# Kernel tuning notes

Hardware: AMD Instinct MI355X
Metric: run time of the kernel (lower is better)

The kernel has to match this reference:

```python
import jax, jax.numpy as jnp
import numpy as np

N_NODES = 100000
N_EDGES = 1600000
IN_F = 128
OUT_F = 128
EDGE_F = 16


def setup_inputs() -> dict:
    key = jax.random.key(0)
    ks = jax.random.split(key, 8)
    H = jax.random.normal(ks[0], (N_NODES, IN_F), dtype=jnp.float32)
    edge_index = jax.random.randint(ks[1], (2, N_EDGES), 0, N_ODES_ := N_NODES, dtype=jnp.int64) if False else jax.random.randint(ks[1], (2, N_EDGES), 0, N_NODES, dtype=jnp.int32).astype(jnp.int64)
    edge_attr = jax.random.normal(ks[2], (N_EDGES, EDGE_F), dtype=jnp.float32)
    We = jax.random.normal(ks[3], (EDGE_F, IN_F), dtype=jnp.float32) * (1.0 / np.sqrt(EDGE_F))
    be = jnp.zeros((IN_F,), dtype=jnp.float32)
    W1 = jax.random.normal(ks[4], (IN_F, OUT_F), dtype=jnp.float32) * (1.0 / np.sqrt(IN_F))
    b1 = jnp.zeros((OUT_F,), dtype=jnp.float32)
    W2 = jax.random.normal(ks[5], (OUT_F, OUT_F), dtype=jnp.float32) * (1.0 / np.sqrt(OUT_F))
    b2 = jnp.zeros((OUT_F,), dtype=jnp.float32)
    return {"H": H, "edge_index": edge_index, "edge_attr": edge_attr,
            "We": We, "be": be, "W1": W1, "b1": b1, "W2": W2, "b2": b2}


def reference(H, edge_index, edge_attr, We, be, W1, b1, W2, b2):
    # edge_mlp: Linear(edge_attr_dim -> in_features)
    edge_messages = edge_attr @ We + be                       # [E, in_f]
    # gather by src, add edge messages
    messages = H[edge_index[0]] + edge_messages               # [E, in_f]
    # scatter_add by dst with dim_size = N
    aggregated = jax.ops.segment_sum(messages, edge_index[1], num_segments=H.shape[0])  # [N, in_f]
    # node_mlp: Linear -> ReLU -> Linear
    h = jax.nn.relu(aggregated @ W1 + b1)                     # [N, out_f]
    out = h @ W2 + b2                                         # [N, out_f]
    return out
```

## Files before the change

kernel.cpp:

```cpp
#include <hip/hip_runtime.h>

#define IN_F 128
#define EF 16

typedef short bf16x8 __attribute__((ext_vector_type(8)));
typedef float f32x4  __attribute__((ext_vector_type(4)));

__device__ __forceinline__ unsigned short f2b(float f) {
    unsigned b = __float_as_uint(f);
    b += 0x7fffu + ((b >> 16) & 1u);
    return (unsigned short)(b >> 16);
}
__device__ __forceinline__ float blo(unsigned u) { return __uint_as_float(u << 16); }
__device__ __forceinline__ float bhi(unsigned u) { return __uint_as_float(u & 0xffff0000u); }


__global__ __launch_bounds__(256) void pre_kernel(
    const float* __restrict__ H, unsigned short* __restrict__ Hb, int n4,
    const int* __restrict__ ei, int* __restrict__ counts,
    int* __restrict__ rank, int E,
    const float* __restrict__ W1, unsigned short* __restrict__ W1t,
    const float* __restrict__ W2, unsigned short* __restrict__ W2t,
    int h2b_blocks, int hist_blocks)
{
    int b = blockIdx.x;
    if (b < h2b_blocks) {
        int i = b * 256 + threadIdx.x;
        if (i < n4) {
            float4 v = ((const float4*)H)[i];
            ushort4 r;
            r.x = f2b(v.x); r.y = f2b(v.y); r.z = f2b(v.z); r.w = f2b(v.w);
            ((ushort4*)Hb)[i] = r;
        }
    } else if (b < h2b_blocks + hist_blocks) {
        int e = (b - h2b_blocks) * 256 + threadIdx.x;
        if (e < E) rank[e] = atomicAdd(&counts[ei[E + e]], 1);
    } else {
        int idx = (b - h2b_blocks - hist_blocks) * 256 + threadIdx.x;
        int w = idx >> 14;
        int r = idx & 16383;
        int n = r >> 7, k = r & 127;
        if (w == 0) W1t[n * IN_F + k] = f2b(W1[k * IN_F + n]);
        else        W2t[n * IN_F + k] = f2b(W2[k * IN_F + n]);
    }
}

__global__ __launch_bounds__(256) void hist_kernel(
    const int* __restrict__ ei, int* __restrict__ counts,
    int* __restrict__ rank, int E)
{
    int e = blockIdx.x * 256 + threadIdx.x;
    if (e >= E) return;
    rank[e] = atomicAdd(&counts[ei[E + e]], 1);
}

__global__ __launch_bounds__(256) void scan_blocks_kernel(
    const int* __restrict__ in, int* __restrict__ out,
    int* __restrict__ partials, int n)
{
    __shared__ int sdata[256];
    const int t = threadIdx.x;
    const int idx0 = blockIdx.x * 1024 + t * 4;
    int v[4];
    #pragma unroll
    for (int i = 0; i < 4; i++) { int idx = idx0 + i; v[i] = (idx < n) ? in[idx] : 0; }
    int s = v[0] + v[1] + v[2] + v[3];
    sdata[t] = s;
    __syncthreads();
    for (int off = 1; off < 256; off <<= 1) {
        int x = (t >= off) ? sdata[t - off] : 0;
        __syncthreads();
        sdata[t] += x;
        __syncthreads();
    }
    if (t == 255) partials[blockIdx.x] = sdata[255];
    int run = (t > 0) ? sdata[t - 1] : 0;
    #pragma unroll
    for (int i = 0; i < 4; i++) {
        int idx = idx0 + i;
        if (idx < n) out[idx] = run;
        run += v[i];
    }
}

__global__ __launch_bounds__(256) void scan_add_fused_kernel(
    int* __restrict__ out, const int* __restrict__ partials, int n)
{
    __shared__ int sw[4];
    const int t = threadIdx.x;
    const int g = blockIdx.x >> 2;
    int v = 0;
    for (int j = t; j < g; j += 256) v += partials[j];
    #pragma unroll
    for (int off = 1; off < 64; off <<= 1) v += __shfl_xor(v, off, 64);
    if ((t & 63) == 0) sw[t >> 6] = v;
    __syncthreads();
    int P = sw[0] + sw[1] + sw[2] + sw[3];
    int idx = blockIdx.x * 256 + t;
    if (idx < n) out[idx] += P;
}

__global__ __launch_bounds__(256) void build_kernel(
    const int* __restrict__ ei, int2* __restrict__ sorted,
    const int* __restrict__ offsets, const int* __restrict__ rank, int E)
{
    int e = blockIdx.x * 256 + threadIdx.x;
    if (e >= E) return;
    int src = ei[e];
    int dst = ei[E + e];
    int pos = offsets[dst] + rank[e];
    sorted[pos] = make_int2(src, e);
}

__global__ __launch_bounds__(256) void gather_fused_kernel(
    const unsigned short* __restrict__ Hb,
    const float* __restrict__ EA,
    const int2* __restrict__ sorted,
    const int* __restrict__ offsets,
    const float* __restrict__ We,
    const float* __restrict__ be,
    unsigned short* __restrict__ Ab,
    int N)
{
    int n = blockIdx.x * 4 + (threadIdx.x >> 6);
    if (n >= N) return;
    int lane = threadIdx.x & 63;
    int half = lane >> 5;
    int l32  = lane & 31;
    int s = offsets[n];
    int e_end = offsets[n + 1];
    float a0 = 0.f, a1 = 0.f, a2 = 0.f, a3 = 0.f, accE = 0.f;
    int i = s + half;
    for (; i + 14 < e_end; i += 16) {
        int2 sE[8];
        #pragma unroll
        for (int j = 0; j < 8; j++) sE[j] = sorted[i + 2 * j];
        uint2 u[8];
        #pragma unroll
        for (int j = 0; j < 8; j++)
            u[j] = *(const uint2*)(Hb + (long long)sE[j].x * IN_F + l32 * 4);
        float ev[8];
        #pragma unroll
        for (int j = 0; j < 8; j++) ev[j] = 0.f;
        if (l32 < EF) {
            #pragma unroll
            for (int j = 0; j < 8; j++) ev[j] = EA[(long long)sE[j].y * EF + l32];
        }
        #pragma unroll
        for (int j = 0; j < 8; j++) {
            a0 += blo(u[j].x); a1 += bhi(u[j].x);
            a2 += blo(u[j].y); a3 += bhi(u[j].y);
            accE += ev[j];
        }
    }
    for (; i + 6 < e_end; i += 8) {
        int2 s0 = sorted[i];
        int2 s1 = sorted[i + 2];
        int2 s2 = sorted[i + 4];
        int2 s3 = sorted[i + 6];
        uint2 u0 = *(const uint2*)(Hb + (long long)s0.x * IN_F + l32 * 4);
        uint2 u1 = *(const uint2*)(Hb + (long long)s1.x * IN_F + l32 * 4);
        uint2 u2 = *(const uint2*)(Hb + (long long)s2.x * IN_F + l32 * 4);
        uint2 u3 = *(const uint2*)(Hb + (long long)s3.x * IN_F + l32 * 4);
        float e0 = 0.f, e1 = 0.f, e2 = 0.f, e3 = 0.f;
        if (l32 < EF) {
            e0 = EA[(long long)s0.y * EF + l32];
            e1 = EA[(long long)s1.y * EF + l32];
            e2 = EA[(long long)s2.y * EF + l32];
            e3 = EA[(long long)s3.y * EF + l32];
        }
        a0 += (blo(u0.x) + blo(u1.x)) + (blo(u2.x) + blo(u3.x));
        a1 += (bhi(u0.x) + bhi(u1.x)) + (bhi(u2.x) + bhi(u3.x));
        a2 += (blo(u0.y) + blo(u1.y)) + (blo(u2.y) + blo(u3.y));
        a3 += (bhi(u0.y) + bhi(u1.y)) + (bhi(u2.y) + bhi(u3.y));
        accE += (e0 + e1) + (e2 + e3);
    }
    for (; i < e_end; i += 2) {
        int2 se = sorted[i];
        uint2 u = *(const uint2*)(Hb + (long long)se.x * IN_F + l32 * 4);
        a0 += blo(u.x); a1 += bhi(u.x); a2 += blo(u.y); a3 += bhi(u.y);
        if (l32 < EF) accE += EA[(long long)se.y * EF + l32];
    }
    a0 += __shfl_xor(a0, 32, 64);
    a1 += __shfl_xor(a1, 32, 64);
    a2 += __shfl_xor(a2, 32, 64);
    a3 += __shfl_xor(a3, 32, 64);
    accE += __shfl_xor(accE, 32, 64);

    const int c4 = l32 * 4;
    const float deg = (float)(e_end - s);
    float4 bev = *(const float4*)&be[c4];
    float vx = a0 + deg * bev.x;
    float vy = a1 + deg * bev.y;
    float vz = a2 + deg * bev.z;
    float vw = a3 + deg * bev.w;
    #pragma unroll
    for (int k = 0; k < EF; k++) {
        float ak = __shfl(accE, k, 64);
        float4 w = *(const float4*)&We[k * IN_F + c4];
        vx += ak * w.x; vy += ak * w.y; vz += ak * w.z; vw += ak * w.w;
    }
    if (half == 0) {
        ushort4 o;
        o.x = f2b(vx); o.y = f2b(vy); o.z = f2b(vz); o.w = f2b(vw);
        *(ushort4*)&Ab[(long long)n * IN_F + c4] = o;
    }
}

__global__ __launch_bounds__(256) void gather_f32_kernel(
    const float* __restrict__ H,
    const float* __restrict__ EA,
    const int2* __restrict__ sorted,
    const int* __restrict__ offsets,
    float* __restrict__ agg,
    float* __restrict__ aggE,
    float* __restrict__ degf,
    int N)
{
    int n = blockIdx.x * 4 + (threadIdx.x >> 6);
    if (n >= N) return;
    int lane = threadIdx.x & 63;
    int half = lane >> 5;
    int l32  = lane & 31;
    int s = offsets[n];
    int e_end = offsets[n + 1];
    float4 acc = make_float4(0.f, 0.f, 0.f, 0.f);
    float accE = 0.f;
    int i = s + half;
    for (; i + 6 < e_end; i += 8) {
        int2 s0 = sorted[i];
        int2 s1 = sorted[i + 2];
        int2 s2 = sorted[i + 4];
        int2 s3 = sorted[i + 6];
        float4 v0 = *(const float4*)(H + (long long)s0.x * IN_F + l32 * 4);
        float4 v1 = *(const float4*)(H + (long long)s1.x * IN_F + l32 * 4);
        float4 v2 = *(const float4*)(H + (long long)s2.x * IN_F + l32 * 4);
        float4 v3 = *(const float4*)(H + (long long)s3.x * IN_F + l32 * 4);
        float e0 = 0.f, e1 = 0.f, e2 = 0.f, e3 = 0.f;
        if (l32 < EF) {
            e0 = EA[(long long)s0.y * EF + l32];
            e1 = EA[(long long)s1.y * EF + l32];
            e2 = EA[(long long)s2.y * EF + l32];
            e3 = EA[(long long)s3.y * EF + l32];
        }
        acc.x += (v0.x + v1.x) + (v2.x + v3.x);
        acc.y += (v0.y + v1.y) + (v2.y + v3.y);
        acc.z += (v0.z + v1.z) + (v2.z + v3.z);
        acc.w += (v0.w + v1.w) + (v2.w + v3.w);
        accE  += (e0 + e1) + (e2 + e3);
    }
    for (; i < e_end; i += 2) {
        int2 se = sorted[i];
        float4 v = *(const float4*)(H + (long long)se.x * IN_F + l32 * 4);
        acc.x += v.x; acc.y += v.y; acc.z += v.z; acc.w += v.w;
        if (l32 < EF) accE += EA[(long long)se.y * EF + l32];
    }
    acc.x += __shfl_xor(acc.x, 32, 64);
    acc.y += __shfl_xor(acc.y, 32, 64);
    acc.z += __shfl_xor(acc.z, 32, 64);
    acc.w += __shfl_xor(acc.w, 32, 64);
    accE  += __shfl_xor(accE, 32, 64);
    if (half == 0) {
        *(float4*)(agg + (long long)n * IN_F + l32 * 4) = acc;
        if (l32 < EF) aggE[n * EF + l32] = accE;
        if (l32 == 0) degf[n] = (float)(e_end - s);
    }
}

__global__ __launch_bounds__(256) void edge_scatter_kernel(
    const float* __restrict__ H,
    const int* __restrict__ ei,
    const float* __restrict__ EA,
    float* __restrict__ agg,
    float* __restrict__ aggE,
    float* __restrict__ deg,
    int E)
{
    long long gid = (long long)blockIdx.x * 256 + threadIdx.x;
    int e = (int)(gid >> 7);
    if (e >= E) return;
    int f = (int)(gid & 127);
    int src = ei[e];
    int dst = ei[E + e];
    float m = H[(long long)src * IN_F + f];
    atomicAdd(&agg[(long long)dst * IN_F + f], m);
    if (f < EF) atomicAdd(&aggE[dst * EF + f], EA[e * EF + f]);
    if (f == 0) atomicAdd(&deg[dst], 1.0f);
}


#define XPITCH 136
__global__ __launch_bounds__(256) void mlp_mfma_kernel(
    const unsigned short* __restrict__ Ab,
    const unsigned short* __restrict__ W1t,
    const unsigned short* __restrict__ W2t,
    const float* __restrict__ b1, const float* __restrict__ b2,
    float* __restrict__ out, int N)
{
    __shared__ unsigned short sW[128 * XPITCH];
    __shared__ unsigned short sX[64 * XPITCH];
    const int t    = threadIdx.x;
    const int tile = blockIdx.x * 64;
    const int lane = t & 63;
    const int wv   = t >> 6;
    const int quad = lane >> 4;
    const int lr   = lane & 15;
    const int M0   = wv * 16;

    {
        const uint4 z = make_uint4(0, 0, 0, 0);
        #pragma unroll
        for (int j = 0; j < 4; j++) {
            int idx = t + 256 * j;
            int row = idx >> 4, c = idx & 15;
            uint4 v = z;
            if (tile + row < N) v = ((const uint4*)Ab)[(long long)(tile + row) * 16 + c];
            ((uint4*)sX)[row * 17 + c] = v;
        }
        #pragma unroll
        for (int j = 0; j < 8; j++) {
            int idx = t + 256 * j;
            int row = idx >> 4, c = idx & 15;
            ((uint4*)sW)[row * 17 + c] = ((const uint4*)W1t)[idx];
        }
    }
    __syncthreads();

    f32x4 acc[8];
    bf16x8 af[4];
    const f32x4 zero = {0.f, 0.f, 0.f, 0.f};

    #pragma unroll
    for (int kt = 0; kt < 4; kt++)
        af[kt] = *(const bf16x8*)&sX[(M0 + lr) * XPITCH + kt * 32 + quad * 8];
    #pragma unroll
    for (int nt = 0; nt < 8; nt++) {
        acc[nt] = zero;
        #pragma unroll
        for (int kt = 0; kt < 4; kt++) {
            bf16x8 bf = *(const bf16x8*)&sW[(nt * 16 + lr) * XPITCH + kt * 32 + quad * 8];
            acc[nt] = __builtin_amdgcn_mfma_f32_16x16x32_bf16(af[kt], bf, acc[nt], 0, 0, 0);
        }
    }
    #pragma unroll
    for (int nt = 0; nt < 8; nt++) {
        int col = nt * 16 + lr;
        float bias = b1[col];
        #pragma unroll
        for (int r = 0; r < 4; r++) {
            float v = fmaxf(acc[nt][r] + bias, 0.f);
            sX[(M0 + quad * 4 + r) * XPITCH + col] = f2b(v);
        }
    }
    __syncthreads();
    #pragma unroll
    for (int j = 0; j < 8; j++) {
        int idx = t + 256 * j;
        int row = idx >> 4, c = idx & 15;
        ((uint4*)sW)[row * 17 + c] = ((const uint4*)W2t)[idx];
    }
    __syncthreads();

    #pragma unroll
    for (int kt = 0; kt < 4; kt++)
        af[kt] = *(const bf16x8*)&sX[(M0 + lr) * XPITCH + kt * 32 + quad * 8];
    #pragma unroll
    for (int nt = 0; nt < 8; nt++) {
        acc[nt] = zero;
        #pragma unroll
        for (int kt = 0; kt < 4; kt++) {
            bf16x8 bf = *(const bf16x8*)&sW[(nt * 16 + lr) * XPITCH + kt * 32 + quad * 8];
            acc[nt] = __builtin_amdgcn_mfma_f32_16x16x32_bf16(af[kt], bf, acc[nt], 0, 0, 0);
        }
    }
    #pragma unroll
    for (int nt = 0; nt < 8; nt++) {
        int col = nt * 16 + lr;
        float bias = b2[col];
        #pragma unroll
        for (int r = 0; r < 4; r++) {
            int row = tile + M0 + quad * 4 + r;
            if (row < N) out[(long long)row * IN_F + col] = acc[nt][r] + bias;
        }
    }
}

__global__ __launch_bounds__(256) void node_mlp_kernel(
    float* agg_out,
    const float* __restrict__ aggE,
    const float* __restrict__ degf,
    const float* __restrict__ We, const float* __restrict__ be,
    const float* __restrict__ W1, const float* __restrict__ b1,
    const float* __restrict__ W2, const float* __restrict__ b2,
    int N)
{
    __shared__ float sA[32][IN_F];
    __shared__ float sH[32][IN_F];
    const int t  = threadIdx.x;
    const int c4 = (t & 31) * 4;
    const int r0 = t >> 5;

    const int tile = blockIdx.x * 32;
    if (tile >= N) return;
    int rows = N - tile;
    if (rows > 32) rows = 32;

    {
        const float4 bev = *(const float4*)&be[c4];
        #pragma unroll
        for (int i = 0; i < 4; i++) {
            int rr = r0 + 8 * i;
            float4 v = make_float4(0.f, 0.f, 0.f, 0.f);
            if (rr < rows) {
                long long r = tile + rr;
                v = *(const float4*)&agg_out[r * IN_F + c4];
                float d = degf[r];
                v.x += d * bev.x; v.y += d * bev.y; v.z += d * bev.z; v.w += d * bev.w;
                #pragma unroll
                for (int k = 0; k < EF; k++) {
                    float a = aggE[r * EF + k];
                    float4 w = *(const float4*)&We[k * IN_F + c4];
                    v.x += a * w.x; v.y += a * w.y; v.z += a * w.z; v.w += a * w.w;
                }
            }
            *(float4*)&sA[rr][c4] = v;
        }
    }
    __syncthreads();
    {
        const float4 bv = *(const float4*)&b1[c4];
        float4 a0 = bv, a1 = bv, a2 = bv, a3 = bv;
        for (int k = 0; k < IN_F; k++) {
            float4 w = *(const float4*)&W1[k * IN_F + c4];
            float x0 = sA[r0][k], x1 = sA[r0 + 8][k], x2 = sA[r0 + 16][k], x3 = sA[r0 + 24][k];
            a0.x += x0 * w.x; a0.y += x0 * w.y; a0.z += x0 * w.z; a0.w += x0 * w.w;
            a1.x += x1 * w.x; a1.y += x1 * w.y; a1.z += x1 * w.z; a1.w += x1 * w.w;
            a2.x += x2 * w.x; a2.y += x2 * w.y; a2.z += x2 * w.z; a2.w += x2 * w.w;
            a3.x += x3 * w.x; a3.y += x3 * w.y; a3.z += x3 * w.z; a3.w += x3 * w.w;
        }
        a0.x = fmaxf(a0.x, 0.f); a0.y = fmaxf(a0.y, 0.f); a0.z = fmaxf(a0.z, 0.f); a0.w = fmaxf(a0.w, 0.f);
        a1.x = fmaxf(a1.x, 0.f); a1.y = fmaxf(a1.y, 0.f); a1.z = fmaxf(a1.z, 0.f); a1.w = fmaxf(a1.w, 0.f);
        a2.x = fmaxf(a2.x, 0.f); a2.y = fmaxf(a2.y, 0.f); a2.z = fmaxf(a2.z, 0.f); a2.w = fmaxf(a2.w, 0.f);
        a3.x = fmaxf(a3.x, 0.f); a3.y = fmaxf(a3.y, 0.f); a3.z = fmaxf(a3.z, 0.f); a3.w = fmaxf(a3.w, 0.f);
        *(float4*)&sH[r0][c4]      = a0;
        *(float4*)&sH[r0 + 8][c4]  = a1;
        *(float4*)&sH[r0 + 16][c4] = a2;
        *(float4*)&sH[r0 + 24][c4] = a3;
    }
    __syncthreads();
    {
        const float4 bv = *(const float4*)&b2[c4];
        float4 a0 = bv, a1 = bv, a2 = bv, a3 = bv;
        for (int k = 0; k < IN_F; k++) {
            float4 w = *(const float4*)&W2[k * IN_F + c4];
            float x0 = sH[r0][k], x1 = sH[r0 + 8][k], x2 = sH[r0 + 16][k], x3 = sH[r0 + 24][k];
            a0.x += x0 * w.x; a0.y += x0 * w.y; a0.z += x0 * w.z; a0.w += x0 * w.w;
            a1.x += x1 * w.x; a1.y += x1 * w.y; a1.z += x1 * w.z; a1.w += x1 * w.w;
            a2.x += x2 * w.x; a2.y += x2 * w.y; a2.z += x2 * w.z; a2.w += x2 * w.w;
            a3.x += x3 * w.x; a3.y += x3 * w.y; a3.z += x3 * w.z; a3.w += x3 * w.w;
        }
        #pragma unroll
        for (int i = 0; i < 4; i++) {
            int rr = r0 + 8 * i;
            if (rr < rows) {
                float4 v = (i == 0) ? a0 : (i == 1) ? a1 : (i == 2) ? a2 : a3;
                *(float4*)&agg_out[(long long)(tile + rr) * IN_F + c4] = v;
            }
        }
    }
}

extern "C" void kernel_launch(void* const* d_in, const int* in_sizes, int n_in,
                              void* d_out, int out_size, void* d_ws, size_t ws_size,
                              hipStream_t stream) {
    const float* H  = (const float*)d_in[0];
    const int*   ei = (const int*)d_in[1];
    const float* EA = (const float*)d_in[2];
    const float* We = (const float*)d_in[3];
    const float* be = (const float*)d_in[4];
    const float* W1 = (const float*)d_in[5];
    const float* b1 = (const float*)d_in[6];
    const float* W2 = (const float*)d_in[7];
    const float* b2 = (const float*)d_in[8];
    float* out = (float*)d_out;

    const int N = in_sizes[0] / IN_F;
    const int E = in_sizes[2] / EF;

    char* p = (char*)d_ws;
    auto alloc = [&](size_t bytes) { char* r = p; p += (bytes + 255) & ~(size_t)255; return r; };
    int2*  sorted   = (int2*)alloc((size_t)E * sizeof(int2));
    int*   rank     = (int*)alloc((size_t)E * sizeof(int));
    float* aggE     = (float*)alloc((size_t)N * EF * sizeof(float));
    float* degf     = (float*)alloc((size_t)N * sizeof(float));
    int*   counts   = (int*)alloc((size_t)(N + 1) * sizeof(int));
    int*   offsets  = (int*)alloc((size_t)(N + 1) * sizeof(int));
    int*   partials = (int*)alloc(1024 * sizeof(int));
    size_t need_base = (size_t)(p - (char*)d_ws);
    unsigned short* Hb = (unsigned short*)alloc((size_t)N * IN_F * sizeof(unsigned short));
    unsigned short* Ab  = (unsigned short*)alloc((size_t)N * IN_F * sizeof(unsigned short));
    unsigned short* W1t = (unsigned short*)alloc((size_t)IN_F * IN_F * sizeof(unsigned short));
    unsigned short* W2t = (unsigned short*)alloc((size_t)IN_F * IN_F * sizeof(unsigned short));
    size_t need_mfma = (size_t)(p - (char*)d_ws);

    const int n_scan = N + 1;
    const int B = (n_scan + 1023) / 1024;

    if (ws_size >= need_mfma && B <= 1024) {
        hipMemsetAsync(counts, 0, (size_t)(N + 1) * sizeof(int), stream);
        const int n4 = N * IN_F / 4;
        const int h2b_blocks  = (n4 + 255) / 256;
        const int hist_blocks = (E + 255) / 256;
        pre_kernel<<<h2b_blocks + hist_blocks + 128, 256, 0, stream>>>(
            H, Hb, n4, ei, counts, rank, E, W1, W1t, W2, W2t, h2b_blocks, hist_blocks);
        scan_blocks_kernel<<<B, 256, 0, stream>>>(counts, offsets, partials, n_scan);
        scan_add_fused_kernel<<<(n_scan + 255) / 256, 256, 0, stream>>>(offsets, partials, n_scan);
        build_kernel<<<(E + 255) / 256, 256, 0, stream>>>(ei, sorted, offsets, rank, E);
        gather_fused_kernel<<<(N + 3) / 4, 256, 0, stream>>>(Hb, EA, sorted, offsets, We, be, Ab, N);
        mlp_mfma_kernel<<<(N + 63) / 64, 256, 0, stream>>>(Ab, W1t, W2t, b1, b2, out, N);
    } else if (ws_size >= need_base && B <= 1024) {
        hipMemsetAsync(counts, 0, (size_t)(N + 1) * sizeof(int), stream);
        hist_kernel<<<(E + 255) / 256, 256, 0, stream>>>(ei, counts, rank, E);
        scan_blocks_kernel<<<B, 256, 0, stream>>>(counts, offsets, partials, n_scan);
        scan_add_fused_kernel<<<(n_scan + 255) / 256, 256, 0, stream>>>(offsets, partials, n_scan);
        build_kernel<<<(E + 255) / 256, 256, 0, stream>>>(ei, sorted, offsets, rank, E);
        gather_f32_kernel<<<(N + 3) / 4, 256, 0, stream>>>(H, EA, sorted, offsets, out, aggE, degf, N);
        node_mlp_kernel<<<(N + 31) / 32, 256, 0, stream>>>(out, aggE, degf, We, be, W1, b1, W2, b2, N);
    } else {
        float* f_aggE = (float*)d_ws;
        float* f_deg  = f_aggE + (size_t)N * EF;
        hipMemsetAsync(d_out, 0, (size_t)N * IN_F * sizeof(float), stream);
        hipMemsetAsync(d_ws, 0, (size_t)N * (EF + 1) * sizeof(float), stream);
        long long tot = (long long)E * IN_F;
        edge_scatter_kernel<<<(int)((tot + 255) / 256), 256, 0, stream>>>(H, ei, EA, out, f_aggE, f_deg, E);
        node_mlp_kernel<<<(N + 31) / 32, 256, 0, stream>>>(out, f_aggE, f_deg, We, be, W1, b1, W2, b2, N);
    }
}
```

Before: 478.3 us.

## Pre-permute edge attributes into dst-sorted order during CSR build

```diff
diff --git a/kernel.cpp b/kernel.cpp
--- a/kernel.cpp
+++ b/kernel.cpp
@@ -100,6 +100,24 @@
     if (idx < n) out[idx] += P;
 }
 
+__global__ __launch_bounds__(256) void build_ea_kernel(
+    const int* __restrict__ ei,
+    const float* __restrict__ EA,
+    const int* __restrict__ offsets, const int* __restrict__ rank,
+    int* __restrict__ sorted_src, float* __restrict__ EAsorted, int E)
+{
+    int e = blockIdx.x * 256 + threadIdx.x;
+    if (e >= E) return;
+    int src = ei[e];
+    int dst = ei[E + e];
+    int pos = offsets[dst] + rank[e];
+    sorted_src[pos] = src;
+    const float4* s4 = (const float4*)(EA + (long long)e * EF);
+    float4* d4 = (float4*)(EAsorted + (long long)pos * EF);
+    float4 v0 = s4[0], v1 = s4[1], v2 = s4[2], v3 = s4[3];
+    d4[0] = v0; d4[1] = v1; d4[2] = v2; d4[3] = v3;
+}
+
 __global__ __launch_bounds__(256) void build_kernel(
     const int* __restrict__ ei, int2* __restrict__ sorted,
     const int* __restrict__ offsets, const int* __restrict__ rank, int E)
@@ -110,6 +128,79 @@
     int dst = ei[E + e];
     int pos = offsets[dst] + rank[e];
     sorted[pos] = make_int2(src, e);
+}
+
+__global__ __launch_bounds__(256) void gather_ea_kernel(
+    const unsigned short* __restrict__ Hb,
+    const float* __restrict__ EAsorted,
+    const int* __restrict__ sorted_src,
+    const int* __restrict__ offsets,
+    const float* __restrict__ We,
+    const float* __restrict__ be,
+    unsigned short* __restrict__ Ab,
+    int N)
+{
+    int n = blockIdx.x * 4 + (threadIdx.x >> 6);
+    if (n >= N) return;
+    int lane = threadIdx.x & 63;
+    int half = lane >> 5;
+    int l32  = lane & 31;
+    int s = offsets[n];
+    int e_end = offsets[n + 1];
+    float a0 = 0.f, a1 = 0.f, a2 = 0.f, a3 = 0.f, accE = 0.f;
+    int i = s + half;
+    for (; i + 6 < e_end; i += 8) {
+        int s0 = sorted_src[i];
+        int s1 = sorted_src[i + 2];
+        int s2 = sorted_src[i + 4];
+        int s3 = sorted_src[i + 6];
+        uint2 u0 = *(const uint2*)(Hb + (long long)s0 * IN_F + l32 * 4);
+        uint2 u1 = *(const uint2*)(Hb + (long long)s1 * IN_F + l32 * 4);
+        uint2 u2 = *(const uint2*)(Hb + (long long)s2 * IN_F + l32 * 4);
+        uint2 u3 = *(const uint2*)(Hb + (long long)s3 * IN_F + l32 * 4);
+        float e0 = 0.f, e1 = 0.f, e2 = 0.f, e3 = 0.f;
+        if (l32 < EF) {
+            e0 = EAsorted[(long long)(i    ) * EF + l32];
+            e1 = EAsorted[(long long)(i + 2) * EF + l32];
+            e2 = EAsorted[(long long)(i + 4) * EF + l32];
+            e3 = EAsorted[(long long)(i + 6) * EF + l32];
+        }
+        a0 += (blo(u0.x) + blo(u1.x)) + (blo(u2.x) + blo(u3.x));
+        a1 += (bhi(u0.x) + bhi(u1.x)) + (bhi(u2.x) + bhi(u3.x));
+        a2 += (blo(u0.y) + blo(u1.y)) + (blo(u2.y) + blo(u3.y));
+        a3 += (bhi(u0.y) + bhi(u1.y)) + (bhi(u2.y) + bhi(u3.y));
+        accE += (e0 + e1) + (e2 + e3);
+    }
+    for (; i < e_end; i += 2) {
+        int se = sorted_src[i];
+        uint2 u = *(const uint2*)(Hb + (long long)se * IN_F + l32 * 4);
+        a0 += blo(u.x); a1 += bhi(u.x); a2 += blo(u.y); a3 += bhi(u.y);
+        if (l32 < EF) accE += EAsorted[(long long)i * EF + l32];
+    }
+    a0 += __shfl_xor(a0, 32, 64);
+    a1 += __shfl_xor(a1, 32, 64);
+    a2 += __shfl_xor(a2, 32, 64);
+    a3 += __shfl_xor(a3, 32, 64);
+    accE += __shfl_xor(accE, 32, 64);
+
+    const int c4 = l32 * 4;
+    const float deg = (float)(e_end - s);
+    float4 bev = *(const float4*)&be[c4];
+    float vx = a0 + deg * bev.x;
+    float vy = a1 + deg * bev.y;
+    float vz = a2 + deg * bev.z;
+    float vw = a3 + deg * bev.w;
+    #pragma unroll
+    for (int k = 0; k < EF; k++) {
+        float ak = __shfl(accE, k, 64);
+        float4 w = *(const float4*)&We[k * IN_F + c4];
+        vx += ak * w.x; vy += ak * w.y; vz += ak * w.z; vw += ak * w.w;
+    }
+    if (half == 0) {
+        ushort4 o;
+        o.x = f2b(vx); o.y = f2b(vy); o.z = f2b(vz); o.w = f2b(vw);
+        *(ushort4*)&Ab[(long long)n * IN_F + c4] = o;
+    }
 }
 
 __global__ __launch_bounds__(256) void gather_fused_kernel(
@@ -131,28 +222,6 @@
     int e_end = offsets[n + 1];
     float a0 = 0.f, a1 = 0.f, a2 = 0.f, a3 = 0.f, accE = 0.f;
     int i = s + half;
-    for (; i + 14 < e_end; i += 16) {
-        int2 sE[8];
-        #pragma unroll
-        for (int j = 0; j < 8; j++) sE[j] = sorted[i + 2 * j];
-        uint2 u[8];
-        #pragma unroll
-        for (int j = 0; j < 8; j++)
-            u[j] = *(const uint2*)(Hb + (long long)sE[j].x * IN_F + l32 * 4);
-        float ev[8];
-        #pragma unroll
-        for (int j = 0; j < 8; j++) ev[j] = 0.f;
-        if (l32 < EF) {
-            #pragma unroll
-            for (int j = 0; j < 8; j++) ev[j] = EA[(long long)sE[j].y * EF + l32];
-        }
-        #pragma unroll
-        for (int j = 0; j < 8; j++) {
-            a0 += blo(u[j].x); a1 += bhi(u[j].x);
-            a2 += blo(u[j].y); a3 += bhi(u[j].y);
-            accE += ev[j];
-        }
-    }
     for (; i + 6 < e_end; i += 8) {
         int2 s0 = sorted[i];
         int2 s1 = sorted[i + 2];
@@ -502,6 +571,9 @@
     unsigned short* W1t = (unsigned short*)alloc((size_t)IN_F * IN_F * sizeof(unsigned short));
     unsigned short* W2t = (unsigned short*)alloc((size_t)IN_F * IN_F * sizeof(unsigned short));
     size_t need_mfma = (size_t)(p - (char*)d_ws);
+    float* EAsorted    = (float*)alloc((size_t)E * EF * sizeof(float));
+    int*   sorted_src  = (int*)alloc((size_t)E * sizeof(int));
+    size_t need_ea = (size_t)(p - (char*)d_ws);
 
     const int n_scan = N + 1;
     const int B = (n_scan + 1023) / 1024;
@@ -515,8 +587,15 @@
             H, Hb, n4, ei, counts, rank, E, W1, W1t, W2, W2t, h2b_blocks, hist_blocks);
         scan_blocks_kernel<<<B, 256, 0, stream>>>(counts, offsets, partials, n_scan);
         scan_add_fused_kernel<<<(n_scan + 255) / 256, 256, 0, stream>>>(offsets, partials, n_scan);
-        build_kernel<<<(E + 255) / 256, 256, 0, stream>>>(ei, sorted, offsets, rank, E);
-        gather_fused_kernel<<<(N + 3) / 4, 256, 0, stream>>>(Hb, EA, sorted, offsets, We, be, Ab, N);
+        if (ws_size >= need_ea) {
+            build_ea_kernel<<<(E + 255) / 256, 256, 0, stream>>>(
+                ei, EA, offsets, rank, sorted_src, EAsorted, E);
+            gather_ea_kernel<<<(N + 3) / 4, 256, 0, stream>>>(
+                Hb, EAsorted, sorted_src, offsets, We, be, Ab, N);
+        } else {
+            build_kernel<<<(E + 255) / 256, 256, 0, stream>>>(ei, sorted, offsets, rank, E);
+            gather_fused_kernel<<<(N + 3) / 4, 256, 0, stream>>>(Hb, EA, sorted, offsets, We, be, Ab, N);
+        }
         mlp_mfma_kernel<<<(N + 63) / 64, 256, 0, stream>>>(Ab, W1t, W2t, b1, b2, out, N);
     } else if (ws_size >= need_base && B <= 1024) {
         hipMemsetAsync(counts, 0, (size_t)(N + 1) * sizeof(int), stream);
```

Result: slower. 517.6 us (+8.2%).

## Scatter edge attributes with atomics and shrink CSR to source indices

Applied to the files above, without the earlier changes.

```diff
diff --git a/kernel.cpp b/kernel.cpp
--- a/kernel.cpp
+++ b/kernel.cpp
@@ -21,6 +21,7 @@
     int* __restrict__ rank, int E,
     const float* __restrict__ W1, unsigned short* __restrict__ W1t,
     const float* __restrict__ W2, unsigned short* __restrict__ W2t,
+    const float* __restrict__ EA, float* __restrict__ aggE,
     int h2b_blocks, int hist_blocks)
 {
     int b = blockIdx.x;
@@ -35,13 +36,21 @@
     } else if (b < h2b_blocks + hist_blocks) {
         int e = (b - h2b_blocks) * 256 + threadIdx.x;
         if (e < E) rank[e] = atomicAdd(&counts[ei[E + e]], 1);
-    } else {
+    } else if (b < h2b_blocks + hist_blocks + 128) {
         int idx = (b - h2b_blocks - hist_blocks) * 256 + threadIdx.x;
         int w = idx >> 14;
         int r = idx & 16383;
         int n = r >> 7, k = r & 127;
         if (w == 0) W1t[n * IN_F + k] = f2b(W1[k * IN_F + n]);
         else        W2t[n * IN_F + k] = f2b(W2[k * IN_F + n]);
+    } else {
+        long long idx = (long long)(b - h2b_blocks - hist_blocks - 128) * 256 + threadIdx.x;
+        if (idx < (long long)E * EF) {
+            int e = (int)(idx >> 4);
+            int f = (int)(idx & 15);
+            int dst = ei[E + e];
+            atomicAdd(&aggE[dst * EF + f], EA[idx]);
+        }
     }
 }
 
@@ -98,6 +107,18 @@
     int P = sw[0] + sw[1] + sw[2] + sw[3];
     int idx = blockIdx.x * 256 + t;
     if (idx < n) out[idx] += P;
+}
+
+__global__ __launch_bounds__(256) void build_src_kernel(
+    const int* __restrict__ ei,
+    const int* __restrict__ offsets, const int* __restrict__ rank,
+    int* __restrict__ sorted_src, int E)
+{
+    int e = blockIdx.x * 256 + threadIdx.x;
+    if (e >= E) return;
+    int dst = ei[E + e];
+    int pos = offsets[dst] + rank[e];
+    sorted_src[pos] = ei[e];
 }
 
 __global__ __launch_bounds__(256) void build_kernel(
@@ -112,11 +133,11 @@
     sorted[pos] = make_int2(src, e);
 }
 
-__global__ __launch_bounds__(256) void gather_fused_kernel(
+__global__ __launch_bounds__(256) void gather_agg_kernel(
     const unsigned short* __restrict__ Hb,
-    const float* __restrict__ EA,
-    const int2* __restrict__ sorted,
+    const int* __restrict__ sorted_src,
     const int* __restrict__ offsets,
+    const float* __restrict__ aggE,
     const float* __restrict__ We,
     const float* __restrict__ be,
     unsigned short* __restrict__ Ab,
@@ -129,63 +150,31 @@
     int l32  = lane & 31;
     int s = offsets[n];
     int e_end = offsets[n + 1];
-    float a0 = 0.f, a1 = 0.f, a2 = 0.f, a3 = 0.f, accE = 0.f;
+    float a0 = 0.f, a1 = 0.f, a2 = 0.f, a3 = 0.f;
     int i = s + half;
-    for (; i + 14 < e_end; i += 16) {
-        int2 sE[8];
-        #pragma unroll
-        for (int j = 0; j < 8; j++) sE[j] = sorted[i + 2 * j];
-        uint2 u[8];
-        #pragma unroll
-        for (int j = 0; j < 8; j++)
-            u[j] = *(const uint2*)(Hb + (long long)sE[j].x * IN_F + l32 * 4);
-        float ev[8];
-        #pragma unroll
-        for (int j = 0; j < 8; j++) ev[j] = 0.f;
-        if (l32 < EF) {
-            #pragma unroll
-            for (int j = 0; j < 8; j++) ev[j] = EA[(long long)sE[j].y * EF + l32];
-        }
-        #pragma unroll
-        for (int j = 0; j < 8; j++) {
-            a0 += blo(u[j].x); a1 += bhi(u[j].x);
-            a2 += blo(u[j].y); a3 += bhi(u[j].y);
-            accE += ev[j];
-        }
-    }
     for (; i + 6 < e_end; i += 8) {
-        int2 s0 = sorted[i];
-        int2 s1 = sorted[i + 2];
-        int2 s2 = sorted[i + 4];
-        int2 s3 = sorted[i + 6];
-        uint2 u0 = *(const uint2*)(Hb + (long long)s0.x * IN_F + l32 * 4);
-        uint2 u1 = *(const uint2*)(Hb + (long long)s1.x * IN_F + l32 * 4);
-        uint2 u2 = *(const uint2*)(Hb + (long long)s2.x * IN_F + l32 * 4);
-        uint2 u3 = *(const uint2*)(Hb + (long long)s3.x * IN_F + l32 * 4);
-        float e0 = 0.f, e1 = 0.f, e2 = 0.f, e3 = 0.f;
-        if (l32 < EF) {
-            e0 = EA[(long long)s0.y * EF + l32];
-            e1 = EA[(long long)s1.y * EF + l32];
-            e2 = EA[(long long)s2.y * EF + l32];
-            e3 = EA[(long long)s3.y * EF + l32];
-        }
+        int s0 = sorted_src[i];
+        int s1 = sorted_src[i + 2];
+        int s2 = sorted_src[i + 4];
+        int s3 = sorted_src[i + 6];
+        uint2 u0 = *(const uint2*)(Hb + (long long)s0 * IN_F + l32 * 4);
+        uint2 u1 = *(const uint2*)(Hb + (long long)s1 * IN_F + l32 * 4);
+        uint2 u2 = *(const uint2*)(Hb + (long long)s2 * IN_F + l32 * 4);
+        uint2 u3 = *(const uint2*)(Hb + (long long)s3 * IN_F + l32 * 4);
         a0 += (blo(u0.x) + blo(u1.x)) + (blo(u2.x) + blo(u3.x));
         a1 += (bhi(u0.x) + bhi(u1.x)) + (bhi(u2.x) + bhi(u3.x));
         a2 += (blo(u0.y) + blo(u1.y)) + (blo(u2.y) + blo(u3.y));
         a3 += (bhi(u0.y) + bhi(u1.y)) + (bhi(u2.y) + bhi(u3.y));
-        accE += (e0 + e1) + (e2 + e3);
     }
     for (; i < e_end; i += 2) {
-        int2 se = sorted[i];
-        uint2 u = *(const uint2*)(Hb + (long long)se.x * IN_F + l32 * 4);
+        int se = sorted_src[i];
+        uint2 u = *(const uint2*)(Hb + (long long)se * IN_F + l32 * 4);
         a0 += blo(u.x); a1 += bhi(u.x); a2 += blo(u.y); a3 += bhi(u.y);
-        if (l32 < EF) accE += EA[(long long)se.y * EF + l32];
     }
     a0 += __shfl_xor(a0, 32, 64);
     a1 += __shfl_xor(a1, 32, 64);
     a2 += __shfl_xor(a2, 32, 64);
     a3 += __shfl_xor(a3, 32, 64);
-    accE += __shfl_xor(accE, 32, 64);
 
     const int c4 = l32 * 4;
     const float deg = (float)(e_end - s);
@@ -196,7 +185,7 @@
     float vw = a3 + deg * bev.w;
     #pragma unroll
     for (int k = 0; k < EF; k++) {
-        float ak = __shfl(accE, k, 64);
+        float ak = aggE[n * EF + k];
         float4 w = *(const float4*)&We[k * IN_F + c4];
         vx += ak * w.x; vy += ak * w.y; vz += ak * w.z; vw += ak * w.w;
     }
@@ -490,9 +479,10 @@
     char* p = (char*)d_ws;
     auto alloc = [&](size_t bytes) { char* r = p; p += (bytes + 255) & ~(size_t)255; return r; };
     int2*  sorted   = (int2*)alloc((size_t)E * sizeof(int2));
+    int*   sorted_src = (int*)sorted;
     int*   rank     = (int*)alloc((size_t)E * sizeof(int));
+    float* degf     = (float*)alloc((size_t)N * sizeof(float));
     float* aggE     = (float*)alloc((size_t)N * EF * sizeof(float));
-    float* degf     = (float*)alloc((size_t)N * sizeof(float));
     int*   counts   = (int*)alloc((size_t)(N + 1) * sizeof(int));
     int*   offsets  = (int*)alloc((size_t)(N + 1) * sizeof(int));
     int*   partials = (int*)alloc(1024 * sizeof(int));
@@ -505,18 +495,23 @@
 
     const int n_scan = N + 1;
     const int B = (n_scan + 1023) / 1024;
+    const size_t zero_bytes = (size_t)((char*)offsets - (char*)aggE);
 
     if (ws_size >= need_mfma && B <= 1024) {
-        hipMemsetAsync(counts, 0, (size_t)(N + 1) * sizeof(int), stream);
+        hipMemsetAsync(aggE, 0, zero_bytes, stream);
         const int n4 = N * IN_F / 4;
         const int h2b_blocks  = (n4 + 255) / 256;
         const int hist_blocks = (E + 255) / 256;
-        pre_kernel<<<h2b_blocks + hist_blocks + 128, 256, 0, stream>>>(
-            H, Hb, n4, ei, counts, rank, E, W1, W1t, W2, W2t, h2b_blocks, hist_blocks);
+        const long long ea_items = (long long)E * EF;
+        const int ea_blocks = (int)((ea_items + 255) / 256);
+        pre_kernel<<<h2b_blocks + hist_blocks + 128 + ea_blocks, 256, 0, stream>>>(
+            H, Hb, n4, ei, counts, rank, E, W1, W1t, W2, W2t, EA, aggE,
+            h2b_blocks, hist_blocks);
         scan_blocks_kernel<<<B, 256, 0, stream>>>(counts, offsets, partials, n_scan);
         scan_add_fused_kernel<<<(n_scan + 255) / 256, 256, 0, stream>>>(offsets, partials, n_scan);
-        build_kernel<<<(E + 255) / 256, 256, 0, stream>>>(ei, sorted, offsets, rank, E);
-        gather_fused_kernel<<<(N + 3) / 4, 256, 0, stream>>>(Hb, EA, sorted, offsets, We, be, Ab, N);
+        build_src_kernel<<<(E + 255) / 256, 256, 0, stream>>>(ei, offsets, rank, sorted_src, E);
+        gather_agg_kernel<<<(N + 3) / 4, 256, 0, stream>>>(
+            Hb, sorted_src, offsets, aggE, We, be, Ab, N);
         mlp_mfma_kernel<<<(N + 63) / 64, 256, 0, stream>>>(Ab, W1t, W2t, b1, b2, out, N);
     } else if (ws_size >= need_base && B <= 1024) {
         hipMemsetAsync(counts, 0, (size_t)(N + 1) * sizeof(int), stream);
```

New measurement: 498.9 us. 1.04x slower.
